# Optimization experiments

Hardware: AMD Instinct MI355X
Metric: run time of the kernel (lower is better)

The kernel has to match this reference:

```python
import jax, jax.numpy as jnp
import numpy as np

TEMPERATURE = 0.07
EPS = 1e-8


def setup_inputs() -> dict:
    key = jax.random.key(0)
    k1, k2 = jax.random.split(key)
    B, D = 8192, 256
    embeddings = jax.random.normal(k1, (B, D), dtype=jnp.float32)
    labels = jax.random.randint(k2, (B,), 0, 6, dtype=jnp.int64)
    return {"embeddings": embeddings, "labels": labels}


def reference(embeddings, labels):
    B = embeddings.shape[0]
    # F.normalize(p=2, dim=1): x / max(||x||, eps)
    norm = jnp.linalg.norm(embeddings, axis=1, keepdims=True)
    en = embeddings / jnp.maximum(norm, 1e-12)
    sim = en @ en.T  # [B, B]
    s = sim / TEMPERATURE

    eye = jnp.eye(B, dtype=bool)
    same = labels[:, None] == labels[None, :]
    pos_mask = same & ~eye            # [B, B]
    neg_mask = (~same) & ~eye         # [B, B]

    exp_s = jnp.exp(s)
    # per-row sum of exp over negatives (matches inner-loop denominator term)
    neg_sum = jnp.sum(jnp.where(neg_mask, exp_s, 0.0), axis=1)  # [B]

    # rows contribute only if they have >=1 positive AND >=1 negative
    row_valid = (pos_mask.sum(axis=1) > 0) & (neg_mask.sum(axis=1) > 0)
    pair_mask = pos_mask & row_valid[:, None]

    # -log( exp(s_ij) / (exp(s_ij) + neg_sum_i + 1e-8) ) per positive pair
    per_pair = -jnp.log(exp_s / (exp_s + neg_sum[:, None] + EPS))
    total = jnp.sum(jnp.where(pair_mask, per_pair, 0.0))
    count = jnp.sum(pair_mask)
    loss = jnp.where(count > 0, total / jnp.maximum(count, 1).astype(total.dtype), 0.0)
    return loss
```

## Files before the change

### kernel.cpp

```cpp
#include <hip/hip_runtime.h>
#include <hip/hip_bf16.h>

#define B_ 8192
#define D_ 256
#define TINV 14.285714285714285f
#define EPS_ 1e-8f
#define BK 32
#define NBLK 32
#define NT 64
#define NTRI (NT*(NT+1)/2)

typedef short short8 __attribute__((ext_vector_type(8)));
typedef float f32x4 __attribute__((ext_vector_type(4)));

__device__ __forceinline__ void mfma_bf16(f32x4& acc, short8 a, short8 b) {
    asm("v_mfma_f32_16x16x32_bf16 %0, %1, %2, %0" : "+v"(acc) : "v"(a), "v"(b));
}

__device__ __forceinline__ void mfma_fence() {
    __builtin_amdgcn_sched_barrier(0);
    asm volatile("s_nop 7\ns_nop 7" ::);
}

__device__ __forceinline__ unsigned short f2bf(float x) {
    __hip_bfloat16 h = __float2bfloat16(x);
    return __builtin_bit_cast(unsigned short, h);
}

__device__ __forceinline__ void tri_decode(int idx, int& bi, int& bj) {
    int t = NTRI - 1 - idx;
    int u = (int)((sqrtf(8.f * (float)t + 1.f) - 1.f) * 0.5f);
    while (u * (u + 1) / 2 > t) --u;
    while ((u + 1) * (u + 2) / 2 <= t) ++u;
    bi = (NT - 1) - u;
    bj = (NT - 1) - (t - u * (u + 1) / 2);
}

__device__ __forceinline__ void stage(const char* gbase, int row0, int k0,
                                      short* ldst, int lane, int wid) {
#pragma unroll
    for (int it = 0; it < 2; ++it) {
        int c = (wid << 1) + it;
        int p = (c << 6) + lane;
        int row = p >> 2;
        int kb = (p & 3) ^ ((row >> 1) & 3);
        const char* g = gbase + ((size_t)(row0 + row) * (D_ * 2) + (size_t)(k0 + kb * 8) * 2);
        __builtin_amdgcn_global_load_lds(
            (const __attribute__((address_space(1))) unsigned int*)g,
            (__attribute__((address_space(3))) unsigned int*)(ldst + (size_t)c * 512),
            16, 0, 0);
    }
}

__device__ __forceinline__ void compute_step(const short* lA, const short* lB,
                                             int lane, int wm, int wn, f32x4 acc[4][4]) {
    int rl = lane & 15, kb = lane >> 4;
    short8 a[4], b[4];
#pragma unroll
    for (int m = 0; m < 4; ++m) {
        int row = wm * 64 + m * 16 + rl;
        a[m] = ((const short8*)lA)[row * 4 + (kb ^ ((row >> 1) & 3))];
    }
#pragma unroll
    for (int n = 0; n < 4; ++n) {
        int row = wn * 64 + n * 16 + rl;
        b[n] = ((const short8*)lB)[row * 4 + (kb ^ ((row >> 1) & 3))];
    }
#pragma unroll
    for (int m = 0; m < 4; ++m)
#pragma unroll
        for (int n = 0; n < 4; ++n)
            mfma_bf16(acc[m][n], a[m], b[n]);
}

__device__ __forceinline__ void gemm_pipe(const char* enb, int i0, int j0,
                                          short (*lA)[128 * BK], short (*lB)[128 * BK],
                                          int lane, int wid, int wm, int wn,
                                          f32x4 acc[4][4]) {
    stage(enb, i0, 0, lA[0], lane, wid);
    stage(enb, j0, 0, lB[0], lane, wid);
#define PIPE_STEP(T)                                                            \
    {                                                                           \
        asm volatile("s_waitcnt vmcnt(0)" ::: "memory");                        \
        __builtin_amdgcn_sched_barrier(0);                                      \
        __builtin_amdgcn_s_barrier();                                           \
        __builtin_amdgcn_sched_barrier(0);                                      \
        if ((T) < 7) {                                                          \
            stage(enb, i0, ((T) + 1) * BK, lA[((T) + 1) & 1], lane, wid);       \
            stage(enb, j0, ((T) + 1) * BK, lB[((T) + 1) & 1], lane, wid);       \
        }                                                                       \
        compute_step(lA[(T) & 1], lB[(T) & 1], lane, wm, wn, acc);              \
    }
    PIPE_STEP(0)
    PIPE_STEP(1)
    PIPE_STEP(2)
    PIPE_STEP(3)
    PIPE_STEP(4)
    PIPE_STEP(5)
    PIPE_STEP(6)
    PIPE_STEP(7)
#undef PIPE_STEP
    mfma_fence();
}

__global__ __launch_bounds__(256) void k_bhist(const int* __restrict__ labels,
                                               unsigned* __restrict__ blockhist,
                                               float* __restrict__ negsum,
                                               float* __restrict__ total) {
    __shared__ unsigned h[8];
    int b = blockIdx.x, t = threadIdx.x;
    if (t < 8) h[t] = 0;
    negsum[b * 256 + t] = 0.f;
    if (b == 0 && t == 0) *total = 0.f;
    __syncthreads();
    atomicAdd(&h[labels[b * 256 + t] & 7], 1u);
    __syncthreads();
    if (t < 8) blockhist[b * 8 + t] = h[t];
}

__global__ __launch_bounds__(256) void k_pos(const int* __restrict__ labels,
                                             const unsigned* __restrict__ blockhist,
                                             unsigned* __restrict__ hist,
                                             int* __restrict__ pos) {
    __shared__ unsigned cnt[8][NBLK];
    __shared__ unsigned clsbase[8];
    __shared__ unsigned wcnt[4][8];
    int b = blockIdx.x, t = threadIdx.x;
    { int bb = t >> 3, c = t & 7; cnt[c][bb] = blockhist[bb * 8 + c]; }
    __syncthreads();
    if (t < 8) {
        unsigned run = 0;
        for (int b2 = 0; b2 < NBLK; ++b2) {
            unsigned v = cnt[t][b2];
            cnt[t][b2] = run;
            run += v;
        }
        clsbase[t] = run;
        if (b == 0) hist[t] = run;
    }
    __syncthreads();
    if (t == 0) {
        unsigned run = 0;
        for (int c = 0; c < 8; ++c) {
            unsigned tot = clsbase[c];
            clsbase[c] = run;
            run += tot;
        }
    }
    __syncthreads();
    int row = b * 256 + t;
    int c = labels[row] & 7;
    int lane = t & 63, w = t >> 6;
    unsigned long long lanebelow = (1ull << lane) - 1ull;
    unsigned myrank = 0;
#pragma unroll
    for (int cv = 0; cv < 8; ++cv) {
        unsigned long long mask = __ballot(c == cv);
        if (lane == 0) wcnt[w][cv] = (unsigned)__popcll(mask);
        if (c == cv) myrank = (unsigned)__popcll(mask & lanebelow);
    }
    __syncthreads();
    unsigned pre = 0;
    for (int wp = 0; wp < 4; ++wp) if (wp < w) pre += wcnt[wp][c];
    pos[row] = (int)(clsbase[c] + cnt[c][b] + pre + myrank);
}

__global__ __launch_bounds__(256) void k_scatter(const float* __restrict__ emb,
                                                 const int* __restrict__ labels,
                                                 const int* __restrict__ pos,
                                                 __hip_bfloat16* __restrict__ en_s,
                                                 int* __restrict__ lab_s) {
    int row = blockIdx.x * 4 + (threadIdx.x >> 6);
    int lane = threadIdx.x & 63;
    float4 v = reinterpret_cast<const float4*>(emb)[(size_t)row * 64 + lane];
    float ss = v.x * v.x + v.y * v.y + v.z * v.z + v.w * v.w;
#pragma unroll
    for (int off = 32; off >= 1; off >>= 1) ss += __shfl_xor(ss, off, 64);
    float scale = 1.0f / fmaxf(sqrtf(ss), 1e-12f);
    int p = pos[row];
    ushort4 o;
    o.x = f2bf(v.x * scale);
    o.y = f2bf(v.y * scale);
    o.z = f2bf(v.z * scale);
    o.w = f2bf(v.w * scale);
    reinterpret_cast<ushort4*>(en_s)[(size_t)p * 64 + lane] = o;
    if (lane == 0) lab_s[p] = labels[row] & 7;
}

template <bool USEP>
__global__ __launch_bounds__(256) void k_negsum(const __hip_bfloat16* __restrict__ en,
                                                const int* __restrict__ lab_s,
                                                float* __restrict__ P,
                                                float* __restrict__ negsum) {
    __shared__ short lA[2][128 * BK];
    __shared__ short lB[2][128 * BK];
    __shared__ int sLi[128], sLj[128];
    int bi, bj;
    tri_decode(blockIdx.x, bi, bj);
    int i0 = bi * 128, j0 = bj * 128;
    int tid = threadIdx.x;
    if (tid < 128) sLi[tid] = lab_s[i0 + tid];
    else           sLj[tid - 128] = lab_s[j0 + tid - 128];
    __syncthreads();

    int lane = tid & 63, wid = tid >> 6;
    int wm = wid >> 1, wn = wid & 1;
    f32x4 acc[4][4] = {};
    gemm_pipe((const char*)en, i0, j0, lA, lB, lane, wid, wm, wn, acc);

    int rl = lane & 15, rowg = (lane >> 4) * 4;
    int lj[4], li[4][4];
#pragma unroll
    for (int n = 0; n < 4; ++n) lj[n] = sLj[wn * 64 + n * 16 + rl];
#pragma unroll
    for (int m = 0; m < 4; ++m)
#pragma unroll
        for (int r = 0; r < 4; ++r) li[m][r] = sLi[wm * 64 + m * 16 + rowg + r];

#pragma unroll
    for (int m = 0; m < 4; ++m)
#pragma unroll
        for (int n = 0; n < 4; ++n)
#pragma unroll
            for (int r = 0; r < 4; ++r)
                acc[m][n][r] = (li[m][r] != lj[n]) ? __expf(acc[m][n][r] * TINV) : 0.f;

    float* sredR = (float*)lA;
    float* sredC = (float*)lB;

#pragma unroll
    for (int m = 0; m < 4; ++m) {
        float part[4];
#pragma unroll
        for (int r = 0; r < 4; ++r)
            part[r] = acc[m][0][r] + acc[m][1][r] + acc[m][2][r] + acc[m][3][r];
#pragma unroll
        for (int off = 1; off < 16; off <<= 1)
#pragma unroll
            for (int r = 0; r < 4; ++r) part[r] += __shfl_xor(part[r], off, 64);
        if (rl == 0) {
#pragma unroll
            for (int r = 0; r < 4; ++r) {
                int row = wm * 64 + m * 16 + rowg + r;
                if (USEP) sredR[wn * 128 + row] = part[r];
                else      atomicAdd(&negsum[i0 + row], part[r]);
            }
        }
    }
    if (bi != bj) {
#pragma unroll
        for (int n = 0; n < 4; ++n) {
            float cp = 0.f;
#pragma unroll
            for (int m = 0; m < 4; ++m)
#pragma unroll
                for (int r = 0; r < 4; ++r) cp += acc[m][n][r];
            cp += __shfl_xor(cp, 16, 64);
            cp += __shfl_xor(cp, 32, 64);
            if (lane < 16) {
                int col = wn * 64 + n * 16 + rl;
                if (USEP) sredC[wm * 128 + col] = cp;
                else      atomicAdd(&negsum[j0 + col], cp);
            }
        }
    }
    if (USEP) {
        __syncthreads();
        if (tid < 128)
            P[(size_t)bj * B_ + i0 + tid] = sredR[tid] + sredR[128 + tid];
        else if (bi != bj)
            P[(size_t)bi * B_ + j0 + (tid - 128)] = sredC[tid - 128] + sredC[128 + (tid - 128)];
    }
}

__global__ __launch_bounds__(256) void k_red(const float* __restrict__ P,
                                             float* __restrict__ negsum) {
    int i = blockIdx.x * 256 + threadIdx.x;
    float s = 0.f;
#pragma unroll 8
    for (int k = 0; k < 64; ++k) s += P[(size_t)k * B_ + i];
    negsum[i] = s;
}

__global__ __launch_bounds__(256) void k_pairs(const __hip_bfloat16* __restrict__ en,
                                               const int* __restrict__ lab_s,
                                               const float* __restrict__ negsum,
                                               const unsigned* __restrict__ hist,
                                               float* __restrict__ total) {
    int bi, bj;
    tri_decode(blockIdx.x, bi, bj);
    int i0 = bi * 128, j0 = bj * 128;
    if (lab_s[j0] > lab_s[i0 + 127]) return;

    __shared__ short lA[2][128 * BK];
    __shared__ short lB[2][128 * BK];
    __shared__ int sLi[128], sLj[128];
    __shared__ float sNgI[128], sNgJ[128];
    int tid = threadIdx.x;
    if (tid < 128) {
        int l = lab_s[i0 + tid];
        unsigned h = hist[l];
        sLi[tid] = (h > 1u && h < (unsigned)B_) ? l : -1;
        sNgI[tid] = negsum[i0 + tid] + EPS_;
    } else {
        int idx = tid - 128;
        int l = lab_s[j0 + idx];
        unsigned h = hist[l];
        sLj[idx] = (h > 1u && h < (unsigned)B_) ? l : -1;
        sNgJ[idx] = negsum[j0 + idx] + EPS_;
    }
    __syncthreads();

    int lane = tid & 63, wid = tid >> 6;
    int wm = wid >> 1, wn = wid & 1;
    f32x4 acc[4][4] = {};
    gemm_pipe((const char*)en, i0, j0, lA, lB, lane, wid, wm, wn, acc);

    int rl = lane & 15, rowg = (lane >> 4) * 4;
    int lj[4];
    float ngJ[4];
#pragma unroll
    for (int n = 0; n < 4; ++n) {
        lj[n] = sLj[wn * 64 + n * 16 + rl];
        ngJ[n] = sNgJ[wn * 64 + n * 16 + rl];
    }

    bool offd = (bi != bj);
    float tot = 0.f;
#pragma unroll
    for (int m = 0; m < 4; ++m) {
#pragma unroll
        for (int r = 0; r < 4; ++r) {
            int ii = wm * 64 + m * 16 + rowg + r;
            int li = sLi[ii];
            float ngI = sNgI[ii];
#pragma unroll
            for (int n = 0; n < 4; ++n) {
                int jj = wn * 64 + n * 16 + rl;
                bool use = (li == lj[n]) && (li >= 0) && (offd || ii != jj);
                if (use) {
                    float s = acc[m][n][r] * TINV;
                    float e = __expf(s);
                    float t = __logf(e + ngI) - s;
                    if (offd) t += __logf(e + ngJ[n]) - s;
                    tot += t;
                }
            }
        }
    }
#pragma unroll
    for (int off = 32; off >= 1; off >>= 1) tot += __shfl_xor(tot, off, 64);
    __shared__ float sred[4];
    if (lane == 0) sred[wid] = tot;
    __syncthreads();
    if (tid == 0) atomicAdd(total, sred[0] + sred[1] + sred[2] + sred[3]);
}

__global__ __launch_bounds__(64) void k_final(const unsigned* __restrict__ hist,
                                              const float* __restrict__ total,
                                              float* __restrict__ out) {
    int t = threadIdx.x;
    unsigned c = 0;
    if (t < 8) {
        unsigned h = hist[t];
        if (h > 1u && h < (unsigned)B_) c = h * (h - 1u);
    }
#pragma unroll
    for (int off = 4; off >= 1; off >>= 1) c += (unsigned)__shfl_xor((int)c, off, 64);
    if (t == 0) out[0] = (c > 0u) ? total[0] / (float)c : 0.f;
}

extern "C" void kernel_launch(void* const* d_in, const int* in_sizes, int n_in,
                              void* d_out, int out_size, void* d_ws, size_t ws_size,
                              hipStream_t stream) {
    const float* emb = (const float*)d_in[0];
    const int* labels = (const int*)d_in[1];
    float* out = (float*)d_out;
    char* ws = (char*)d_ws;

    const size_t EN_BYTES = (size_t)B_ * D_ * 2;
    __hip_bfloat16* en_s = (__hip_bfloat16*)ws;
    char* p = ws + EN_BYTES;
    float* negsum = (float*)p;            p += (size_t)B_ * 4;
    int* lab_s = (int*)p;                 p += (size_t)B_ * 4;
    int* pos = (int*)p;                   p += (size_t)B_ * 4;
    unsigned* blockhist = (unsigned*)p;   p += NBLK * 8 * 4;
    unsigned* hist = (unsigned*)p;        p += 64;
    float* total = (float*)p;             p += 64;
    float* P = (float*)p;
    size_t need = (size_t)(p - ws) + (size_t)NT * B_ * 4;
    bool bigws = ws_size >= need;

    k_bhist<<<NBLK, 256, 0, stream>>>(labels, blockhist, negsum, total);
    k_pos<<<NBLK, 256, 0, stream>>>(labels, blockhist, hist, pos);
    k_scatter<<<B_ / 4, 256, 0, stream>>>(emb, labels, pos, en_s, lab_s);
    if (bigws) {
        k_negsum<true><<<NTRI, 256, 0, stream>>>(en_s, lab_s, P, negsum);
        k_red<<<B_ / 256, 256, 0, stream>>>(P, negsum);
    } else {
        k_negsum<false><<<NTRI, 256, 0, stream>>>(en_s, lab_s, P, negsum);
    }
    k_pairs<<<NTRI, 256, 0, stream>>>(en_s, lab_s, negsum, hist, total);
    k_final<<<1, 64, 0, stream>>>(hist, total, out);
}
```

Before: 79.45 us.

## Replace negsum GEMM with 256x256 register-resident A tiles and direct atomics

Replaces the 128x128 triangular negsum kernel and its partial-sum reduction pass with a 256x256 tile kernel. Each wave keeps its 64 A rows for the full K=256 in registers and streams B in 64-row chunks through double-buffered, swizzled LDS. Row sums and column sums of the masked exp go to negsum through atomics, which removes the P buffer and the k_red launch. The cost is heavy register pressure from holding A and accumulators, fewer blocks (528), and uneven work on diagonal tiles.

```diff
diff --git a/kernel.cpp b/kernel.cpp
--- a/kernel.cpp
+++ b/kernel.cpp
@@ -9,6 +9,8 @@
 #define NBLK 32
 #define NT 64
 #define NTRI (NT*(NT+1)/2)
+#define NT2 32
+#define NTRI2 (NT2*(NT2+1)/2)
 
 typedef short short8 __attribute__((ext_vector_type(8)));
 typedef float f32x4 __attribute__((ext_vector_type(4)));
@@ -27,13 +29,148 @@
     return __builtin_bit_cast(unsigned short, h);
 }
 
-__device__ __forceinline__ void tri_decode(int idx, int& bi, int& bj) {
-    int t = NTRI - 1 - idx;
+__device__ __forceinline__ void tri_decode_n(int idx, int N, int& bi, int& bj) {
+    int ntri = N * (N + 1) / 2;
+    int t = ntri - 1 - idx;
     int u = (int)((sqrtf(8.f * (float)t + 1.f) - 1.f) * 0.5f);
     while (u * (u + 1) / 2 > t) --u;
     while ((u + 1) * (u + 2) / 2 <= t) ++u;
-    bi = (NT - 1) - u;
-    bj = (NT - 1) - (t - u * (u + 1) / 2);
+    bi = (N - 1) - u;
+    bj = (N - 1) - (t - u * (u + 1) / 2);
+}
+
+
+__device__ __forceinline__ void stageB(const char* gbase, int jbase,
+                                       short* ldst, int tid) {
+#pragma unroll
+    for (int it = 0; it < 8; ++it) {
+        int p = it * 256 + tid;
+        int row = p >> 5, pos = p & 31;
+        int c = (pos - row) & 31;
+        const char* g = gbase + ((size_t)(jbase + row) * 512 + (size_t)c * 16);
+        __builtin_amdgcn_global_load_lds(
+            (const __attribute__((address_space(1))) unsigned int*)g,
+            (__attribute__((address_space(3))) unsigned int*)(ldst + (size_t)p * 8),
+            16, 0, 0);
+    }
+}
+
+__global__ __launch_bounds__(256, 2) void k_gemm(const __hip_bfloat16* __restrict__ en,
+                                                 const int* __restrict__ lab_s,
+                                                 float* __restrict__ negsum) {
+    __shared__ short lB[2][64 * 256];
+    __shared__ float colred[2][256];
+    __shared__ int sLj[256];
+
+    int bi, bj;
+    tri_decode_n(blockIdx.x, NT2, bi, bj);
+    int i0 = bi * 256, j0 = bj * 256;
+    int tid = threadIdx.x, lane = tid & 63, w = tid >> 6;
+    int rl = lane & 15, kb = lane >> 4;
+    const char* enb = (const char*)en;
+
+    stageB(enb, j0, lB[0], tid);
+    stageB(enb, j0 + 64, lB[1], tid);
+
+    int arow = i0 + w * 64;
+    short8 a[4][8];
+#pragma unroll
+    for (int m = 0; m < 4; ++m) {
+        const char* rp = enb + (size_t)(arow + m * 16 + rl) * 512 + (size_t)kb * 16;
+#pragma unroll
+        for (int s = 0; s < 8; ++s)
+            a[m][s] = *(const short8*)(rp + s * 64);
+    }
+    unsigned liP[4];
+#pragma unroll
+    for (int m = 0; m < 4; ++m) {
+        unsigned v = 0;
+#pragma unroll
+        for (int r = 0; r < 4; ++r)
+            v |= ((unsigned)lab_s[arow + m * 16 + kb * 4 + r] & 7u) << (8 * r);
+        liP[m] = v;
+    }
+    sLj[tid] = lab_s[j0 + tid];
+
+    float rsum[4][4] = {};
+    __syncthreads();
+
+#pragma unroll
+    for (int t = 0; t < 4; ++t) {
+        bool active = (bi != bj) || (t >= w);
+        f32x4 acc[4][4] = {};
+        float cp[4] = {0.f, 0.f, 0.f, 0.f};
+        if (active) {
+            const short8* bt = (const short8*)lB[t & 1];
+#pragma unroll
+            for (int s = 0; s < 8; ++s) {
+                short8 b[4];
+#pragma unroll
+                for (int n = 0; n < 4; ++n) {
+                    int row = n * 16 + rl;
+                    int pos = (s * 4 + kb + row) & 31;
+                    b[n] = bt[row * 32 + pos];
+                }
+#pragma unroll
+                for (int m = 0; m < 4; ++m)
+#pragma unroll
+                    for (int n = 0; n < 4; ++n)
+                        mfma_bf16(acc[m][n], a[m][s], b[n]);
+            }
+            mfma_fence();
+            int lj[4];
+#pragma unroll
+            for (int n = 0; n < 4; ++n) lj[n] = sLj[t * 64 + n * 16 + rl];
+#pragma unroll
+            for (int m = 0; m < 4; ++m) {
+#pragma unroll
+                for (int r = 0; r < 4; ++r) {
+                    int li = (int)((liP[m] >> (8 * r)) & 255u);
+                    float rs = 0.f;
+#pragma unroll
+                    for (int n = 0; n < 4; ++n) {
+                        float e = (li != lj[n]) ? __expf(acc[m][n][r] * TINV) : 0.f;
+                        rs += e;
+                        cp[n] += e;
+                    }
+                    rsum[m][r] += rs;
+                }
+            }
+#pragma unroll
+            for (int n = 0; n < 4; ++n) {
+                cp[n] += __shfl_xor(cp[n], 16, 64);
+                cp[n] += __shfl_xor(cp[n], 32, 64);
+            }
+        }
+        bool docol = (bi != bj) || (t > w);
+        if (lane < 16) {
+#pragma unroll
+            for (int n = 0; n < 4; ++n)
+                colred[t & 1][w * 64 + n * 16 + lane] = docol ? cp[n] : 0.f;
+        }
+        __syncthreads();
+        if (tid < 64) {
+            const float* cr = colred[t & 1];
+            float c = cr[tid] + cr[64 + tid] + cr[128 + tid] + cr[192 + tid];
+            atomicAdd(&negsum[j0 + t * 64 + tid], c);
+        }
+        if (t + 2 < 4) stageB(enb, j0 + (t + 2) * 64, lB[t & 1], tid);
+    }
+
+#pragma unroll
+    for (int off = 1; off < 16; off <<= 1)
+#pragma unroll
+        for (int m = 0; m < 4; ++m)
+#pragma unroll
+            for (int r = 0; r < 4; ++r)
+                rsum[m][r] += __shfl_xor(rsum[m][r], off, 64);
+    if (rl == 0) {
+#pragma unroll
+        for (int m = 0; m < 4; ++m)
+#pragma unroll
+            for (int r = 0; r < 4; ++r)
+                atomicAdd(&negsum[arow + m * 16 + kb * 4 + r], rsum[m][r]);
+    }
 }
 
 __device__ __forceinline__ void stage(const char* gbase, int row0, int k0,
@@ -187,108 +324,13 @@
     if (lane == 0) lab_s[p] = labels[row] & 7;
 }
 
-template <bool USEP>
-__global__ __launch_bounds__(256) void k_negsum(const __hip_bfloat16* __restrict__ en,
-                                                const int* __restrict__ lab_s,
-                                                float* __restrict__ P,
-                                                float* __restrict__ negsum) {
-    __shared__ short lA[2][128 * BK];
-    __shared__ short lB[2][128 * BK];
-    __shared__ int sLi[128], sLj[128];
-    int bi, bj;
-    tri_decode(blockIdx.x, bi, bj);
-    int i0 = bi * 128, j0 = bj * 128;
-    int tid = threadIdx.x;
-    if (tid < 128) sLi[tid] = lab_s[i0 + tid];
-    else           sLj[tid - 128] = lab_s[j0 + tid - 128];
-    __syncthreads();
-
-    int lane = tid & 63, wid = tid >> 6;
-    int wm = wid >> 1, wn = wid & 1;
-    f32x4 acc[4][4] = {};
-    gemm_pipe((const char*)en, i0, j0, lA, lB, lane, wid, wm, wn, acc);
-
-    int rl = lane & 15, rowg = (lane >> 4) * 4;
-    int lj[4], li[4][4];
-#pragma unroll
-    for (int n = 0; n < 4; ++n) lj[n] = sLj[wn * 64 + n * 16 + rl];
-#pragma unroll
-    for (int m = 0; m < 4; ++m)
-#pragma unroll
-        for (int r = 0; r < 4; ++r) li[m][r] = sLi[wm * 64 + m * 16 + rowg + r];
-
-#pragma unroll
-    for (int m = 0; m < 4; ++m)
-#pragma unroll
-        for (int n = 0; n < 4; ++n)
-#pragma unroll
-            for (int r = 0; r < 4; ++r)
-                acc[m][n][r] = (li[m][r] != lj[n]) ? __expf(acc[m][n][r] * TINV) : 0.f;
-
-    float* sredR = (float*)lA;
-    float* sredC = (float*)lB;
-
-#pragma unroll
-    for (int m = 0; m < 4; ++m) {
-        float part[4];
-#pragma unroll
-        for (int r = 0; r < 4; ++r)
-            part[r] = acc[m][0][r] + acc[m][1][r] + acc[m][2][r] + acc[m][3][r];
-#pragma unroll
-        for (int off = 1; off < 16; off <<= 1)
-#pragma unroll
-            for (int r = 0; r < 4; ++r) part[r] += __shfl_xor(part[r], off, 64);
-        if (rl == 0) {
-#pragma unroll
-            for (int r = 0; r < 4; ++r) {
-                int row = wm * 64 + m * 16 + rowg + r;
-                if (USEP) sredR[wn * 128 + row] = part[r];
-                else      atomicAdd(&negsum[i0 + row], part[r]);
-            }
-        }
-    }
-    if (bi != bj) {
-#pragma unroll
-        for (int n = 0; n < 4; ++n) {
-            float cp = 0.f;
-#pragma unroll
-            for (int m = 0; m < 4; ++m)
-#pragma unroll
-                for (int r = 0; r < 4; ++r) cp += acc[m][n][r];
-            cp += __shfl_xor(cp, 16, 64);
-            cp += __shfl_xor(cp, 32, 64);
-            if (lane < 16) {
-                int col = wn * 64 + n * 16 + rl;
-                if (USEP) sredC[wm * 128 + col] = cp;
-                else      atomicAdd(&negsum[j0 + col], cp);
-            }
-        }
-    }
-    if (USEP) {
-        __syncthreads();
-        if (tid < 128)
-            P[(size_t)bj * B_ + i0 + tid] = sredR[tid] + sredR[128 + tid];
-        else if (bi != bj)
-            P[(size_t)bi * B_ + j0 + (tid - 128)] = sredC[tid - 128] + sredC[128 + (tid - 128)];
-    }
-}
-
-__global__ __launch_bounds__(256) void k_red(const float* __restrict__ P,
-                                             float* __restrict__ negsum) {
-    int i = blockIdx.x * 256 + threadIdx.x;
-    float s = 0.f;
-#pragma unroll 8
-    for (int k = 0; k < 64; ++k) s += P[(size_t)k * B_ + i];
-    negsum[i] = s;
-}
-
 __global__ __launch_bounds__(256) void k_pairs(const __hip_bfloat16* __restrict__ en,
                                                const int* __restrict__ lab_s,
                                                const float* __restrict__ negsum,
                                                const unsigned* __restrict__ hist,
                                                float* __restrict__ total) {
     int bi, bj;
-    tri_decode(blockIdx.x, bi, bj);
+    tri_decode_n(blockIdx.x, NT, bi, bj);
     int i0 = bi * 128, j0 = bj * 128;
     if (lab_s[j0] > lab_s[i0 + 127]) return;
 
@@ -387,19 +429,11 @@
     unsigned* blockhist = (unsigned*)p;   p += NBLK * 8 * 4;
     unsigned* hist = (unsigned*)p;        p += 64;
     float* total = (float*)p;             p += 64;
-    float* P = (float*)p;
-    size_t need = (size_t)(p - ws) + (size_t)NT * B_ * 4;
-    bool bigws = ws_size >= need;
 
     k_bhist<<<NBLK, 256, 0, stream>>>(labels, blockhist, negsum, total);
     k_pos<<<NBLK, 256, 0, stream>>>(labels, blockhist, hist, pos);
     k_scatter<<<B_ / 4, 256, 0, stream>>>(emb, labels, pos, en_s, lab_s);
-    if (bigws) {
-        k_negsum<true><<<NTRI, 256, 0, stream>>>(en_s, lab_s, P, negsum);
-        k_red<<<B_ / 256, 256, 0, stream>>>(P, negsum);
-    } else {
-        k_negsum<false><<<NTRI, 256, 0, stream>>>(en_s, lab_s, P, negsum);
-    }
+    k_gemm<<<NTRI2, 256, 0, stream>>>(en_s, lab_s, negsum);
     k_pairs<<<NTRI, 256, 0, stream>>>(en_s, lab_s, negsum, hist, total);
     k_final<<<1, 64, 0, stream>>>(hist, total, out);
 }
```

Result: slower. 95.90 us (+20.7%).
